# Performance work log

Hardware: AMD Instinct MI355X
Metric: run time of the kernel (lower is better)

Reference implementation:

```python
import jax, jax.numpy as jnp
import numpy as np

B, S0, S1 = 4, 768, 256
T = S0 + S1
D0, D1 = 2048, 1024
N, K, H = 8, 1, 256  # num_heads, num_kv_heads, head_dim
G = N // K
BIG_NEG = -2.3819763e38


def _apply_rope(x, positions, max_wavelength=10000):
    # x: [B, L, Hn, Hd]; positions: [B, L] float32
    half = x.shape[-1] // 2
    freq_exponents = (2.0 / x.shape[-1]) * jnp.arange(half, dtype=jnp.float32)
    timescale = max_wavelength ** freq_exponents
    radians = positions[..., None] / timescale[None, None, :]   # [B, L, half]
    radians = radians[..., None, :]                             # [B, L, 1, half]
    sin, cos = jnp.sin(radians), jnp.cos(radians)
    x1, x2 = jnp.split(x, 2, axis=-1)
    res = jnp.concatenate([x1 * cos - x2 * sin, x2 * cos + x1 * sin], axis=-1)
    return res.astype(x.dtype)


def setup_inputs() -> dict:
    key = jax.random.key(0)
    ks = jax.random.split(key, 8)
    x0 = jax.random.normal(ks[0], (B, S0, D0), dtype=jnp.float32)
    x1 = jax.random.normal(ks[1], (B, S1, D1), dtype=jnp.float32)
    positions = jnp.broadcast_to(jnp.arange(T, dtype=jnp.float32), (B, T))
    # causal mask [B, 1, T, T]
    attn_mask = jnp.broadcast_to(jnp.tril(jnp.ones((T, T), dtype=bool)), (B, 1, T, T))
    # lecun_normal-style init: std = 1/sqrt(fan_in=width)
    q0_w = jax.random.normal(ks[2], (N, D0, H), dtype=jnp.float32) * (D0 ** -0.5)
    kv0_w = jax.random.normal(ks[3], (2, K, D0, H), dtype=jnp.float32) * (D0 ** -0.5)
    q1_w = jax.random.normal(ks[4], (N, D1, H), dtype=jnp.float32) * (D1 ** -0.5)
    kv1_w = jax.random.normal(ks[5], (2, K, D1, H), dtype=jnp.float32) * (D1 ** -0.5)
    o0_w = jax.random.normal(ks[6], (N, H, D0), dtype=jnp.float32) * ((N * H) ** -0.5)
    o1_w = jax.random.normal(ks[7], (N, H, D1), dtype=jnp.float32) * ((N * H) ** -0.5)
    return {"x0": x0, "x1": x1, "positions": positions, "attn_mask": attn_mask,
            "q0_w": q0_w, "kv0_w": kv0_w, "q1_w": q1_w, "kv1_w": kv1_w,
            "o0_w": o0_w, "o1_w": o1_w}


def reference(x0, x1, positions, attn_mask, q0_w, kv0_w, q1_w, kv1_w, o0_w, o1_w):
    dtype = x0.dtype
    # per-stream GQA projections (num_kv_heads != num_heads path)
    q_a = jnp.einsum('BTD,NDH->BTNH', x0, q0_w)
    kv_a = jnp.einsum('BSD,CKDH->CBSKH', x0, kv0_w)
    q_b = jnp.einsum('BTD,NDH->BTNH', x1, q1_w)
    kv_b = jnp.einsum('BSD,CKDH->CBSKH', x1, kv1_w)
    # concat streams along sequence
    q = jnp.concatenate([q_a, q_b], axis=1)                 # [B, T, N, H]
    k = jnp.concatenate([kv_a[0], kv_b[0]], axis=1)         # [B, T, K, H]
    v = jnp.concatenate([kv_a[1], kv_b[1]], axis=1)         # [B, T, K, H]
    # inline RoPE + query scaling
    q = _apply_rope(q, positions) * (H ** -0.5)
    k = _apply_rope(k, positions)
    # GQA grouping: N = K * G
    qg = q.reshape(q.shape[0], q.shape[1], K, G, H)          # [B, T, K, G, H]
    logits = jnp.einsum('BTKGH,BSKH->BKGTS', qg, k,
                        preferred_element_type=jnp.float32)  # fp32 scores
    masked = jnp.where(attn_mask[:, :, None, :, :], logits, BIG_NEG)
    probs = jax.nn.softmax(masked, axis=-1).astype(dtype)
    encoded = jnp.einsum('BKGTS,BSKH->BTKGH', probs, v)
    encoded = encoded.reshape(encoded.shape[0], encoded.shape[1], N, H)  # [B, T, N, H]
    out0 = jnp.einsum('BTNH,NHD->BTD', encoded[:, :S0], o0_w)
    out1 = jnp.einsum('BTNH,NHD->BTD', encoded[:, S0:], o1_w)
    return (out0, out1)
```

## Files before the change

kernel.cpp:

```cpp
#include <hip/hip_runtime.h>

typedef unsigned short u16;
typedef __attribute__((ext_vector_type(8))) short bf16x8;
typedef __attribute__((ext_vector_type(4))) float f32x4;

#define CB   4
#define CS0  768
#define CS1  256
#define CT   1024
#define CD0  2048
#define CD1  1024
#define CN   8
#define CH   256
#define IDENT (1 << 30)
#define BIGBASE 0x7fffffff

__device__ __forceinline__ float bf2f(u16 u) {
    union { unsigned int i; float f; } v;
    v.i = ((unsigned int)u) << 16;
    return v.f;
}
__device__ __forceinline__ u16 f2bf(float f) {
    union { float f; unsigned int i; } v;
    v.f = f;
    unsigned int r = 0x7fffu + ((v.i >> 16) & 1u);
    return (u16)((v.i + r) >> 16);
}

__device__ __forceinline__ void gl_lds16(const u16* g, u16* lds_base) {
    __builtin_amdgcn_global_load_lds(
        (const __attribute__((address_space(1))) void*)g,
        (__attribute__((address_space(3))) void*)lds_base,
        16, 0, 0);
}

struct PSeg { const float* in; u16* out; int R, C, base, lgx, lgy, mode; };
struct PSeg8 { PSeg t[8]; };

__global__ __launch_bounds__(256) void prep_multi(PSeg8 segs)
{
    __shared__ float tl[32][33];
    int bid = blockIdx.x;
    PSeg g = segs.t[0];
    #pragma unroll
    for (int i = 1; i < 8; i++)
        if (bid >= segs.t[i].base) g = segs.t[i];
    int r = bid - g.base;
    if (g.mode == 0) {
        int i = r * 256 + threadIdx.x;
        float4 v = ((const float4*)g.in)[i];
        ushort4 o;
        o.x = f2bf(v.x); o.y = f2bf(v.y); o.z = f2bf(v.z); o.w = f2bf(v.w);
        ((ushort4*)g.out)[i] = o;
    } else {
        int bx = r & ((1 << g.lgx) - 1);
        int by = (r >> g.lgx) & ((1 << g.lgy) - 1);
        int bz = r >> (g.lgx + g.lgy);
        const float* in = g.in + (size_t)bz * g.R * g.C;
        u16* out = g.out + (size_t)bz * g.R * g.C;
        int c0 = bx * 32, r0 = by * 32;
        int tx = threadIdx.x & 31, ty = threadIdx.x >> 5;
        #pragma unroll
        for (int i = 0; i < 32; i += 8)
            tl[ty + i][tx] = in[(size_t)(r0 + ty + i) * g.C + c0 + tx];
        __syncthreads();
        #pragma unroll
        for (int i = 0; i < 32; i += 8)
            out[(size_t)(c0 + ty + i) * g.R + r0 + tx] = f2bf(tl[tx][ty + i]);
    }
}

struct GSeg {
    const u16* A; const u16* BT; void* C;
    int K, Cstride, base, lgnx;
    int Sa, Ta, ta, Sc, Tc, tc, obf, pad;
};
struct GSeg4 { GSeg s[4]; };

__global__ __launch_bounds__(256) void mfma_gemm_multi(GSeg4 segs)
{
    __shared__ u16 As[128 * 32];
    __shared__ u16 Bs[128 * 32];

    int bid = blockIdx.x;
    GSeg g = segs.s[0];
    if (bid >= segs.s[1].base) g = segs.s[1];
    if (bid >= segs.s[2].base) g = segs.s[2];
    if (bid >= segs.s[3].base) g = segs.s[3];

    int tid  = threadIdx.x;
    int r    = bid - g.base;
    int n0   = (r & ((1 << g.lgnx) - 1)) * 128;
    int m0   = (r >> g.lgnx) * 128;
    int wave = tid >> 6, lane = tid & 63;

    int srow  = tid >> 2;
    int skoff = ((tid & 3) ^ ((srow >> 1) & 3)) * 8;
    int am1 = m0 + srow, am2 = m0 + 64 + srow;
    const u16* aptr1 = g.A + (size_t)((am1 / g.Sa) * g.Ta + g.ta + am1 % g.Sa) * g.K + skoff;
    const u16* aptr2 = g.A + (size_t)((am2 / g.Sa) * g.Ta + g.ta + am2 % g.Sa) * g.K + skoff;
    const u16* bptr1 = g.BT + (size_t)(n0 + srow) * g.K + skoff;
    const u16* bptr2 = g.BT + (size_t)(n0 + 64 + srow) * g.K + skoff;

    int mw = (wave >> 1) * 64, nw = (wave & 1) * 64;
    int lrow = lane & 15;
    int q4   = lane >> 4;
    int sw   = (q4 ^ ((lrow >> 1) & 3)) * 8;

    f32x4 acc[4][4] = {};

    for (int k0 = 0; k0 < g.K; k0 += 32) {
        gl_lds16(aptr1 + k0, As + wave * 512);
        gl_lds16(aptr2 + k0, As + 2048 + wave * 512);
        gl_lds16(bptr1 + k0, Bs + wave * 512);
        gl_lds16(bptr2 + k0, Bs + 2048 + wave * 512);
        __syncthreads();
        bf16x8 af[4], bfr[4];
        #pragma unroll
        for (int i = 0; i < 4; i++)
            af[i] = *(const bf16x8*)&As[(mw + i * 16 + lrow) * 32 + sw];
        #pragma unroll
        for (int i = 0; i < 4; i++)
            bfr[i] = *(const bf16x8*)&Bs[(nw + i * 16 + lrow) * 32 + sw];
        #pragma unroll
        for (int mi = 0; mi < 4; mi++)
            #pragma unroll
            for (int ni = 0; ni < 4; ni++)
                acc[mi][ni] = __builtin_amdgcn_mfma_f32_16x16x32_bf16(
                    af[mi], bfr[ni], acc[mi][ni], 0, 0, 0);
        __syncthreads();
    }

    #pragma unroll
    for (int mi = 0; mi < 4; mi++) {
        #pragma unroll
        for (int rr = 0; rr < 4; rr++) {
            int mm = m0 + mw + mi * 16 + q4 * 4 + rr;
            int grow = (mm / g.Sc) * g.Tc + g.tc + mm % g.Sc;
            if (g.obf) {
                u16* crow = (u16*)g.C + (size_t)grow * g.Cstride + n0 + nw + lrow;
                #pragma unroll
                for (int ni = 0; ni < 4; ni++)
                    crow[ni * 16] = f2bf(acc[mi][ni][rr]);
            } else {
                float* crow = (float*)g.C + (size_t)grow * g.Cstride + n0 + nw + lrow;
                #pragma unroll
                for (int ni = 0; ni < 4; ni++)
                    crow[ni * 16] = acc[mi][ni][rr];
            }
        }
    }
}

__global__ __launch_bounds__(256) void rope_vt_kernel(
    const u16* __restrict__ qsrc, const u16* __restrict__ kvsrc,
    const float* __restrict__ positions,
    u16* __restrict__ qb, u16* __restrict__ kb, u16* __restrict__ vto)
{
    int bid = blockIdx.x;
    if (bid < 18432) {
        int idx = bid * 256 + threadIdx.x;
        const int QP = CB * CT * CN * 128;
        if (idx < QP) {
            int h  = idx & 127;
            int n  = (idx >> 7) & 7;
            int bt = idx >> 10;
            const u16* base = qsrc + (size_t)bt * 2048 + n * 256;
            float pos = positions[bt];
            float ts  = powf(10000.0f, (float)h * (1.0f / 128.0f));
            float rr  = pos / ts;
            float sn = sinf(rr), cs = cosf(rr);
            float x1 = bf2f(base[h]), x2 = bf2f(base[h + 128]);
            u16* ob = qb + (size_t)bt * 2048 + n * 256;
            ob[h]       = f2bf((x1 * cs - x2 * sn) * 0.0625f);
            ob[h + 128] = f2bf((x2 * cs + x1 * sn) * 0.0625f);
        } else {
            int j  = idx - QP;
            int h  = j & 127;
            int bt = j >> 7;
            const u16* base = kvsrc + (size_t)bt * 512;
            float pos = positions[bt];
            float ts  = powf(10000.0f, (float)h * (1.0f / 128.0f));
            float rr  = pos / ts;
            float sn = sinf(rr), cs = cosf(rr);
            float x1 = bf2f(base[h]), x2 = bf2f(base[h + 128]);
            int b = bt >> 10, t = bt & 1023;
            int h2 = h + 128;
            kb[((size_t)(b * 8 + (h  >> 5)) * 1024 + t) * 32 + (h  & 31)] = f2bf(x1 * cs - x2 * sn);
            kb[((size_t)(b * 8 + (h2 >> 5)) * 1024 + t) * 32 + (h2 & 31)] = f2bf(x2 * cs + x1 * sn);
        }
    } else {
        int vb = bid - 18432;
        int h  = threadIdx.x;
        int sc = vb & 31;
        int b  = vb >> 5;
        const u16* src = kvsrc + ((size_t)(b * 1024 + sc * 32) * 512 + 256 + h);
        u16* dst = vto + ((size_t)(b * 32 + sc) * 256 + h) * 32;
        u16 buf[32];
        #pragma unroll
        for (int ss = 0; ss < 32; ss++)
            buf[ss] = src[(size_t)ss * 512];
        #pragma unroll
        for (int i = 0; i < 8; i++)
            ((ushort4*)dst)[i] = ((ushort4*)buf)[i];
    }
}

__global__ __launch_bounds__(256) void flash_attn(
    const u16* __restrict__ qb, const u16* __restrict__ kb,
    const u16* __restrict__ vt, u16* __restrict__ encoded)
{
    __shared__ __align__(16) u16 Ks[8 * 64 * 32];
    __shared__ __align__(16) u16 Vs[2 * 256 * 32];
    __shared__ __align__(16) u16 Pw[4][16 * 72];

    int tid  = threadIdx.x;
    int wave = tid >> 6, lane = tid & 63;
    int q4 = lane >> 4, l15 = lane & 15;
    int swz = (q4 ^ ((l15 >> 1) & 3)) * 8;

    int bid  = blockIdx.x;
    int half = bid >> 8;
    int r    = bid & 255;
    int b    = (half << 1) | (r >> 7);
    int ti   = r & 127;
    if (half) ti = 127 - ti;
    int t0 = ti * 8;

    bf16x8 af[8];
    {
        int m = wave * 16 + l15;
        int head = m >> 3, tl = m & 7;
        const u16* qrow = qb + ((size_t)(b * CT + t0 + tl) * 2048 + head * 256 + q4 * 8);
        #pragma unroll
        for (int kc = 0; kc < 8; kc++)
            af[kc] = *(const bf16x8*)(qrow + kc * 32);
    }

    f32x4 O[16] = {};
    float lrun[4] = {0.f, 0.f, 0.f, 0.f};

    int send = t0 + 8;
    for (int s0 = 0; s0 < send; s0 += 64) {
        bool lastTile = (s0 + 64 >= send);
        if (s0) __syncthreads();
        #pragma unroll
        for (int is = 0; is < 8; is++) {
            int ubase = is * 256 + wave * 64;
            int u = ubase + lane;
            int s = (u >> 2) & 63, hc = u >> 8;
            int ug = (u & 3) ^ ((s >> 1) & 3);
            const u16* g = kb + ((size_t)((b * 8 + hc) * 1024 + s0 + s) * 32 + ug * 8);
            gl_lds16(g, Ks + (size_t)ubase * 8);
        }
        #pragma unroll
        for (int is = 0; is < 8; is++) {
            int ubase = is * 256 + wave * 64;
            int u = ubase + lane;
            int h = (u >> 2) & 255;
            int vg = (u & 3) ^ ((h >> 1) & 3);
            const u16* g = vt + ((size_t)(b * 32 + (s0 >> 5)) * 8192 + (size_t)(u >> 2) * 32 + vg * 8);
            gl_lds16(g, Vs + (size_t)ubase * 8);
        }
        __syncthreads();

        f32x4 P[4];
        #pragma unroll
        for (int ni = 0; ni < 4; ni++) {
            f32x4 c = {};
            #pragma unroll
            for (int kc = 0; kc < 8; kc++) {
                bf16x8 bfr = *(const bf16x8*)&Ks[kc * 2048 + (ni * 16 + l15) * 32 + swz];
                c = __builtin_amdgcn_mfma_f32_16x16x32_bf16(af[kc], bfr, c, 0, 0, 0);
            }
            P[ni] = c;
        }

        if (lastTile) {
            #pragma unroll
            for (int ni = 0; ni < 4; ni++)
                #pragma unroll
                for (int rr = 0; rr < 4; rr++) {
                    int trow = t0 + ((q4 * 4 + rr) & 7);
                    int scol = s0 + ni * 16 + l15;
                    if (scol > trow) P[ni][rr] = -3.0e38f;
                }
        }

        #pragma unroll
        for (int ni = 0; ni < 4; ni++)
            #pragma unroll
            for (int rr = 0; rr < 4; rr++) {
                float e = __expf(P[ni][rr]);
                P[ni][rr] = e;
                Pw[wave][(q4 * 4 + rr) * 72 + ni * 16 + l15] = f2bf(e);
            }
        #pragma unroll
        for (int rr = 0; rr < 4; rr++) {
            float s = (P[0][rr] + P[1][rr]) + (P[2][rr] + P[3][rr]);
            s += __shfl_xor(s, 1);
            s += __shfl_xor(s, 2);
            s += __shfl_xor(s, 4);
            s += __shfl_xor(s, 8);
            lrun[rr] += s;
        }

        bf16x8 pa0 = *(const bf16x8*)&Pw[wave][l15 * 72 + q4 * 8];
        bf16x8 pa1 = *(const bf16x8*)&Pw[wave][l15 * 72 + 32 + q4 * 8];
        #pragma unroll
        for (int nc = 0; nc < 16; nc++) {
            bf16x8 b0 = *(const bf16x8*)&Vs[(nc * 16 + l15) * 32 + swz];
            bf16x8 b1 = *(const bf16x8*)&Vs[8192 + (nc * 16 + l15) * 32 + swz];
            O[nc] = __builtin_amdgcn_mfma_f32_16x16x32_bf16(pa0, b0, O[nc], 0, 0, 0);
            O[nc] = __builtin_amdgcn_mfma_f32_16x16x32_bf16(pa1, b1, O[nc], 0, 0, 0);
        }
    }

    #pragma unroll
    for (int rr = 0; rr < 4; rr++) {
        int mm = wave * 16 + q4 * 4 + rr;
        int hd = mm >> 3, tl = mm & 7;
        u16* erow = encoded + ((size_t)(b * CT + t0 + tl) * 2048 + hd * 256 + l15);
        float inv = 1.0f / lrun[rr];
        #pragma unroll
        for (int nc = 0; nc < 16; nc++)
            erow[nc * 16] = f2bf(O[nc][rr] * inv);
    }
}

extern "C" void kernel_launch(void* const* d_in, const int* in_sizes, int n_in,
                              void* d_out, int out_size, void* d_ws, size_t ws_size,
                              hipStream_t stream)
{
    const float* x0        = (const float*)d_in[0];
    const float* x1        = (const float*)d_in[1];
    const float* positions = (const float*)d_in[2];
    const float* q0_w  = (const float*)d_in[4];
    const float* kv0_w = (const float*)d_in[5];
    const float* q1_w  = (const float*)d_in[6];
    const float* kv1_w = (const float*)d_in[7];
    const float* o0_w  = (const float*)d_in[8];
    const float* o1_w  = (const float*)d_in[9];
    float* out = (float*)d_out;

    char* W = (char*)d_ws;
    u16* qbuf16  = (u16*)(W);
    u16* kvbuf16 = (u16*)(W + 16777216);
    u16* WTo0  = (u16*)(W + 20971520);
    u16* WTo1  = (u16*)(W + 29360128);
    u16* x0b   = (u16*)(W + 33554432);
    u16* x1b   = (u16*)(W + 46137344);
    u16* WTq0  = (u16*)(W + 48234496);
    u16* WTkv0 = (u16*)(W + 56623104);
    u16* WTq1  = (u16*)(W + 58720256);
    u16* WTkv1 = (u16*)(W + 62914560);
    u16* qb  = x0b;
    u16* kb  = WTkv0;
    u16* vtb = WTq1;
    u16* encoded = qbuf16;

    PSeg8 ps8;
    ps8.t[0] = { x0,    x0b,      0,    0,     0, 0, 0, 0 };
    ps8.t[1] = { x1,    x1b,      0,    0,  6144, 0, 0, 0 };
    ps8.t[2] = { q0_w,  WTq0,  2048,  256,  7168, 3, 6, 1 };
    ps8.t[3] = { kv0_w, WTkv0, 2048,  256, 11264, 3, 6, 1 };
    ps8.t[4] = { q1_w,  WTq1,  1024,  256, 12288, 3, 5, 1 };
    ps8.t[5] = { kv1_w, WTkv1, 1024,  256, 14336, 3, 5, 1 };
    ps8.t[6] = { o0_w,  WTo0,  2048, 2048, 14848, 6, 6, 1 };
    ps8.t[7] = { o1_w,  WTo1,  2048, 1024, 18944, 5, 6, 1 };
    prep_multi<<<dim3(20992), dim3(256), 0, stream>>>(ps8);

    GSeg4 ps;
    ps.s[0] = { x0b, WTq0,  qbuf16,  2048, 2048,   0, 4, IDENT, 0, 0, CS0, CT, 0,   1, 0 };
    ps.s[1] = { x0b, WTkv0, kvbuf16, 2048,  512, 384, 2, IDENT, 0, 0, CS0, CT, 0,   1, 0 };
    ps.s[2] = { x1b, WTq1,  qbuf16,  1024, 2048, 480, 4, IDENT, 0, 0, CS1, CT, CS0, 1, 0 };
    ps.s[3] = { x1b, WTkv1, kvbuf16, 1024,  512, 608, 2, IDENT, 0, 0, CS1, CT, CS0, 1, 0 };
    mfma_gemm_multi<<<dim3(640), dim3(256), 0, stream>>>(ps);

    rope_vt_kernel<<<dim3(18560), dim3(256), 0, stream>>>(
        qbuf16, kvbuf16, positions, qb, kb, vtb);

    flash_attn<<<dim3(512), dim3(256), 0, stream>>>(qb, kb, vtb, encoded);

    GSeg4 os;
    os.s[0] = { encoded, WTo0, out, 2048, 2048,   0, 4, CS0, CT, 0,   IDENT, 0, 0, 0, 0 };
    os.s[1] = { encoded, WTo1, out + (size_t)CB * CS0 * CD0,
                2048, 1024, 384, 3, CS1, CT, CS0, IDENT, 0, 0, 0, 0 };
    os.s[2] = { nullptr, nullptr, nullptr, 0, 0, BIGBASE, 0, 1, 0, 0, 1, 0, 0, 0, 0 };
    os.s[3] = { nullptr, nullptr, nullptr, 0, 0, BIGBASE, 0, 1, 0, 0, 1, 0, 0, 0, 0 };
    mfma_gemm_multi<<<dim3(448), dim3(256), 0, stream>>>(os);
}
```

Before: 330.0 us.

## Fuse all stages into one persistent kernel with grid barriers

Replaces the five separate launches (convert/transpose, QKV GEMM, RoPE/V-transpose, flash attention, output GEMM) with a single persistent kernel of 512 blocks. The blocks loop over each stage's work items and synchronise through a software grid barrier in workspace memory. It also precomputes the RoPE timescales in LDS, switches to fast sin/cos intrinsics, and remaps GEMM tile order. The intent is to remove launch gaps and tail effects between stages. In exchange, the barriers serialise all blocks, shared memory is sized for the largest stage which may cap occupancy, and co-residency of all 512 blocks is assumed.

```diff
diff --git a/kernel.cpp b/kernel.cpp
--- a/kernel.cpp
+++ b/kernel.cpp
@@ -10,10 +10,9 @@
 #define CT   1024
 #define CD0  2048
 #define CD1  1024
-#define CN   8
-#define CH   256
 #define IDENT (1 << 30)
-#define BIGBASE 0x7fffffff
+#define NBLK 512u
+#define BAR_OFF (64u * 1024u * 1024u)
 
 __device__ __forceinline__ float bf2f(u16 u) {
     union { unsigned int i; float f; } v;
@@ -26,7 +25,6 @@
     unsigned int r = 0x7fffu + ((v.i >> 16) & 1u);
     return (u16)((v.i + r) >> 16);
 }
-
 __device__ __forceinline__ void gl_lds16(const u16* g, u16* lds_base) {
     __builtin_amdgcn_global_load_lds(
         (const __attribute__((address_space(1))) void*)g,
@@ -34,73 +32,50 @@
         16, 0, 0);
 }
 
-struct PSeg { const float* in; u16* out; int R, C, base, lgx, lgy, mode; };
-struct PSeg8 { PSeg t[8]; };
-
-__global__ __launch_bounds__(256) void prep_multi(PSeg8 segs)
+__device__ __forceinline__ void grid_barrier(unsigned* bar) {
+    __syncthreads();
+    __threadfence();
+    if (threadIdx.x == 0) {
+        unsigned* cnt = bar;
+        unsigned* gen = bar + 16;
+        unsigned g = __hip_atomic_load(gen, __ATOMIC_RELAXED, __HIP_MEMORY_SCOPE_AGENT);
+        unsigned a = __hip_atomic_fetch_add(cnt, 1u, __ATOMIC_ACQ_REL, __HIP_MEMORY_SCOPE_AGENT);
+        if (a == NBLK - 1u) {
+            __hip_atomic_store(cnt, 0u, __ATOMIC_RELAXED, __HIP_MEMORY_SCOPE_AGENT);
+            __hip_atomic_store(gen, g + 1u, __ATOMIC_RELEASE, __HIP_MEMORY_SCOPE_AGENT);
+        } else {
+            while (__hip_atomic_load(gen, __ATOMIC_ACQUIRE, __HIP_MEMORY_SCOPE_AGENT) == g)
+                __builtin_amdgcn_s_sleep(2);
+        }
+    }
+    __syncthreads();
+    __threadfence();
+}
+
+struct KArgs {
+    const float *x0, *x1, *positions, *q0w, *kv0w, *q1w, *kv1w, *o0w, *o1w;
+    float* out;
+    u16 *x0b, *x1b, *WTq0, *WTkv0, *WTq1, *WTkv1, *WTo0, *WTo1;
+    u16 *qbuf16, *kvbuf16;
+    unsigned* bar;
+};
+
+__device__ __forceinline__ void gemm_tile(
+    const u16* __restrict__ A, const u16* __restrict__ BT, void* C, int obf,
+    int K, int Cstride, int m0, int n0,
+    int Sa, int Ta, int ta, int Sc, int Tc, int tc,
+    u16* As, u16* Bs)
 {
-    __shared__ float tl[32][33];
-    int bid = blockIdx.x;
-    PSeg g = segs.t[0];
-    #pragma unroll
-    for (int i = 1; i < 8; i++)
-        if (bid >= segs.t[i].base) g = segs.t[i];
-    int r = bid - g.base;
-    if (g.mode == 0) {
-        int i = r * 256 + threadIdx.x;
-        float4 v = ((const float4*)g.in)[i];
-        ushort4 o;
-        o.x = f2bf(v.x); o.y = f2bf(v.y); o.z = f2bf(v.z); o.w = f2bf(v.w);
-        ((ushort4*)g.out)[i] = o;
-    } else {
-        int bx = r & ((1 << g.lgx) - 1);
-        int by = (r >> g.lgx) & ((1 << g.lgy) - 1);
-        int bz = r >> (g.lgx + g.lgy);
-        const float* in = g.in + (size_t)bz * g.R * g.C;
-        u16* out = g.out + (size_t)bz * g.R * g.C;
-        int c0 = bx * 32, r0 = by * 32;
-        int tx = threadIdx.x & 31, ty = threadIdx.x >> 5;
-        #pragma unroll
-        for (int i = 0; i < 32; i += 8)
-            tl[ty + i][tx] = in[(size_t)(r0 + ty + i) * g.C + c0 + tx];
-        __syncthreads();
-        #pragma unroll
-        for (int i = 0; i < 32; i += 8)
-            out[(size_t)(c0 + ty + i) * g.R + r0 + tx] = f2bf(tl[tx][ty + i]);
-    }
-}
-
-struct GSeg {
-    const u16* A; const u16* BT; void* C;
-    int K, Cstride, base, lgnx;
-    int Sa, Ta, ta, Sc, Tc, tc, obf, pad;
-};
-struct GSeg4 { GSeg s[4]; };
-
-__global__ __launch_bounds__(256) void mfma_gemm_multi(GSeg4 segs)
-{
-    __shared__ u16 As[128 * 32];
-    __shared__ u16 Bs[128 * 32];
-
-    int bid = blockIdx.x;
-    GSeg g = segs.s[0];
-    if (bid >= segs.s[1].base) g = segs.s[1];
-    if (bid >= segs.s[2].base) g = segs.s[2];
-    if (bid >= segs.s[3].base) g = segs.s[3];
-
     int tid  = threadIdx.x;
-    int r    = bid - g.base;
-    int n0   = (r & ((1 << g.lgnx) - 1)) * 128;
-    int m0   = (r >> g.lgnx) * 128;
     int wave = tid >> 6, lane = tid & 63;
 
     int srow  = tid >> 2;
     int skoff = ((tid & 3) ^ ((srow >> 1) & 3)) * 8;
     int am1 = m0 + srow, am2 = m0 + 64 + srow;
-    const u16* aptr1 = g.A + (size_t)((am1 / g.Sa) * g.Ta + g.ta + am1 % g.Sa) * g.K + skoff;
-    const u16* aptr2 = g.A + (size_t)((am2 / g.Sa) * g.Ta + g.ta + am2 % g.Sa) * g.K + skoff;
-    const u16* bptr1 = g.BT + (size_t)(n0 + srow) * g.K + skoff;
-    const u16* bptr2 = g.BT + (size_t)(n0 + 64 + srow) * g.K + skoff;
+    const u16* aptr1 = A + (size_t)((am1 / Sa) * Ta + ta + am1 % Sa) * K + skoff;
+    const u16* aptr2 = A + (size_t)((am2 / Sa) * Ta + ta + am2 % Sa) * K + skoff;
+    const u16* bptr1 = BT + (size_t)(n0 + srow) * K + skoff;
+    const u16* bptr2 = BT + (size_t)(n0 + 64 + srow) * K + skoff;
 
     int mw = (wave >> 1) * 64, nw = (wave & 1) * 64;
     int lrow = lane & 15;
@@ -109,7 +84,7 @@
 
     f32x4 acc[4][4] = {};
 
-    for (int k0 = 0; k0 < g.K; k0 += 32) {
+    for (int k0 = 0; k0 < K; k0 += 32) {
         gl_lds16(aptr1 + k0, As + wave * 512);
         gl_lds16(aptr2 + k0, As + 2048 + wave * 512);
         gl_lds16(bptr1 + k0, Bs + wave * 512);
@@ -136,14 +111,14 @@
         #pragma unroll
         for (int rr = 0; rr < 4; rr++) {
             int mm = m0 + mw + mi * 16 + q4 * 4 + rr;
-            int grow = (mm / g.Sc) * g.Tc + g.tc + mm % g.Sc;
-            if (g.obf) {
-                u16* crow = (u16*)g.C + (size_t)grow * g.Cstride + n0 + nw + lrow;
+            int grow = (mm / Sc) * Tc + tc + mm % Sc;
+            if (obf) {
+                u16* crow = (u16*)C + (size_t)grow * Cstride + n0 + nw + lrow;
                 #pragma unroll
                 for (int ni = 0; ni < 4; ni++)
                     crow[ni * 16] = f2bf(acc[mi][ni][rr]);
             } else {
-                float* crow = (float*)g.C + (size_t)grow * g.Cstride + n0 + nw + lrow;
+                float* crow = (float*)C + (size_t)grow * Cstride + n0 + nw + lrow;
                 #pragma unroll
                 for (int ni = 0; ni < 4; ni++)
                     crow[ni * 16] = acc[mi][ni][rr];
@@ -152,179 +127,268 @@
     }
 }
 
-__global__ __launch_bounds__(256) void rope_vt_kernel(
-    const u16* __restrict__ qsrc, const u16* __restrict__ kvsrc,
-    const float* __restrict__ positions,
-    u16* __restrict__ qb, u16* __restrict__ kb, u16* __restrict__ vto)
+__device__ __forceinline__ void tile_coords(int r, int nt, int mt, int& m0, int& n0)
 {
+    int wr = (r & 7) * (nt >> 3) + (r >> 3);
+    m0 = (wr % mt) * 128;
+    n0 = (wr / mt) * 128;
+}
+
+__global__ __launch_bounds__(256, 2) void mega(KArgs a)
+{
+    __shared__ __align__(16) char smem[74752];
+    int tid = threadIdx.x;
     int bid = blockIdx.x;
-    if (bid < 18432) {
-        int idx = bid * 256 + threadIdx.x;
-        const int QP = CB * CT * CN * 128;
-        if (idx < QP) {
-            int h  = idx & 127;
-            int n  = (idx >> 7) & 7;
-            int bt = idx >> 10;
-            const u16* base = qsrc + (size_t)bt * 2048 + n * 256;
-            float pos = positions[bt];
-            float ts  = powf(10000.0f, (float)h * (1.0f / 128.0f));
-            float rr  = pos / ts;
-            float sn = sinf(rr), cs = cosf(rr);
-            float x1 = bf2f(base[h]), x2 = bf2f(base[h + 128]);
-            u16* ob = qb + (size_t)bt * 2048 + n * 256;
-            ob[h]       = f2bf((x1 * cs - x2 * sn) * 0.0625f);
-            ob[h + 128] = f2bf((x2 * cs + x1 * sn) * 0.0625f);
-        } else {
-            int j  = idx - QP;
-            int h  = j & 127;
-            int bt = j >> 7;
-            const u16* base = kvsrc + (size_t)bt * 512;
-            float pos = positions[bt];
-            float ts  = powf(10000.0f, (float)h * (1.0f / 128.0f));
-            float rr  = pos / ts;
-            float sn = sinf(rr), cs = cosf(rr);
-            float x1 = bf2f(base[h]), x2 = bf2f(base[h + 128]);
-            int b = bt >> 10, t = bt & 1023;
-            int h2 = h + 128;
-            kb[((size_t)(b * 8 + (h  >> 5)) * 1024 + t) * 32 + (h  & 31)] = f2bf(x1 * cs - x2 * sn);
-            kb[((size_t)(b * 8 + (h2 >> 5)) * 1024 + t) * 32 + (h2 & 31)] = f2bf(x2 * cs + x1 * sn);
-        }
-    } else {
-        int vb = bid - 18432;
-        int h  = threadIdx.x;
-        int sc = vb & 31;
-        int b  = vb >> 5;
-        const u16* src = kvsrc + ((size_t)(b * 1024 + sc * 32) * 512 + 256 + h);
-        u16* dst = vto + ((size_t)(b * 32 + sc) * 256 + h) * 32;
-        u16 buf[32];
-        #pragma unroll
-        for (int ss = 0; ss < 32; ss++)
-            buf[ss] = src[(size_t)ss * 512];
-        #pragma unroll
-        for (int i = 0; i < 8; i++)
-            ((ushort4*)dst)[i] = ((ushort4*)buf)[i];
-    }
-}
-
-__global__ __launch_bounds__(256) void flash_attn(
-    const u16* __restrict__ qb, const u16* __restrict__ kb,
-    const u16* __restrict__ vt, u16* __restrict__ encoded)
-{
-    __shared__ __align__(16) u16 Ks[8 * 64 * 32];
-    __shared__ __align__(16) u16 Vs[2 * 256 * 32];
-    __shared__ __align__(16) u16 Pw[4][16 * 72];
-
-    int tid  = threadIdx.x;
-    int wave = tid >> 6, lane = tid & 63;
-    int q4 = lane >> 4, l15 = lane & 15;
-    int swz = (q4 ^ ((l15 >> 1) & 3)) * 8;
-
-    int bid  = blockIdx.x;
-    int half = bid >> 8;
-    int r    = bid & 255;
-    int b    = (half << 1) | (r >> 7);
-    int ti   = r & 127;
-    if (half) ti = 127 - ti;
-    int t0 = ti * 8;
-
-    bf16x8 af[8];
+
     {
-        int m = wave * 16 + l15;
-        int head = m >> 3, tl = m & 7;
-        const u16* qrow = qb + ((size_t)(b * CT + t0 + tl) * 2048 + head * 256 + q4 * 8);
-        #pragma unroll
-        for (int kc = 0; kc < 8; kc++)
-            af[kc] = *(const bf16x8*)(qrow + kc * 32);
-    }
-
-    f32x4 O[16] = {};
-    float lrun[4] = {0.f, 0.f, 0.f, 0.f};
-
-    int send = t0 + 8;
-    for (int s0 = 0; s0 < send; s0 += 64) {
-        bool lastTile = (s0 + 64 >= send);
-        if (s0) __syncthreads();
-        #pragma unroll
-        for (int is = 0; is < 8; is++) {
-            int ubase = is * 256 + wave * 64;
-            int u = ubase + lane;
-            int s = (u >> 2) & 63, hc = u >> 8;
-            int ug = (u & 3) ^ ((s >> 1) & 3);
-            const u16* g = kb + ((size_t)((b * 8 + hc) * 1024 + s0 + s) * 32 + ug * 8);
-            gl_lds16(g, Ks + (size_t)ubase * 8);
-        }
-        #pragma unroll
-        for (int is = 0; is < 8; is++) {
-            int ubase = is * 256 + wave * 64;
-            int u = ubase + lane;
-            int h = (u >> 2) & 255;
-            int vg = (u & 3) ^ ((h >> 1) & 3);
-            const u16* g = vt + ((size_t)(b * 32 + (s0 >> 5)) * 8192 + (size_t)(u >> 2) * 32 + vg * 8);
-            gl_lds16(g, Vs + (size_t)ubase * 8);
-        }
+        float (*tl)[33] = (float(*)[33])smem;
+        for (int u = bid; u < 20992; u += NBLK) {
+            const float* in; u16* outp; int R=0, C=0, lgx=0, lgy=0, mode, base;
+            if      (u <  6144) { in=a.x0;   outp=a.x0b;   mode=0; base=0; }
+            else if (u <  7168) { in=a.x1;   outp=a.x1b;   mode=0; base=6144; }
+            else if (u < 11264) { in=a.q0w;  outp=a.WTq0;  R=2048; C=256;  lgx=3; lgy=6; mode=1; base=7168; }
+            else if (u < 12288) { in=a.kv0w; outp=a.WTkv0; R=2048; C=256;  lgx=3; lgy=6; mode=1; base=11264; }
+            else if (u < 14336) { in=a.q1w;  outp=a.WTq1;  R=1024; C=256;  lgx=3; lgy=5; mode=1; base=12288; }
+            else if (u < 14848) { in=a.kv1w; outp=a.WTkv1; R=1024; C=256;  lgx=3; lgy=5; mode=1; base=14336; }
+            else if (u < 18944) { in=a.o0w;  outp=a.WTo0;  R=2048; C=2048; lgx=6; lgy=6; mode=1; base=14848; }
+            else                { in=a.o1w;  outp=a.WTo1;  R=2048; C=1024; lgx=5; lgy=6; mode=1; base=18944; }
+            int r = u - base;
+            if (mode == 0) {
+                int i = r * 256 + tid;
+                float4 v = ((const float4*)in)[i];
+                ushort4 o;
+                o.x = f2bf(v.x); o.y = f2bf(v.y); o.z = f2bf(v.z); o.w = f2bf(v.w);
+                ((ushort4*)outp)[i] = o;
+            } else {
+                int bx = r & ((1 << lgx) - 1);
+                int by = (r >> lgx) & ((1 << lgy) - 1);
+                int bz = r >> (lgx + lgy);
+                const float* inz = in + (size_t)bz * R * C;
+                u16* outz = outp + (size_t)bz * R * C;
+                int c0 = bx * 32, r0 = by * 32;
+                int tx = tid & 31, ty = tid >> 5;
+                __syncthreads();
+                #pragma unroll
+                for (int i = 0; i < 32; i += 8)
+                    tl[ty + i][tx] = inz[(size_t)(r0 + ty + i) * C + c0 + tx];
+                __syncthreads();
+                #pragma unroll
+                for (int i = 0; i < 32; i += 8)
+                    outz[(size_t)(c0 + ty + i) * R + r0 + tx] = f2bf(tl[tx][ty + i]);
+            }
+        }
+    }
+    grid_barrier(a.bar);
+
+    {
+        u16* As = (u16*)smem;
+        u16* Bs = (u16*)(smem + 8192);
+        for (int t = bid; t < 640; t += NBLK) {
+            const u16 *A, *BT; u16* C; int K, Cst, base, nt, mt, Sc, Tc, tc;
+            if      (t < 384) { A=a.x0b; BT=a.WTq0;  C=a.qbuf16;  K=2048; Cst=2048; base=0;   nt=384; mt=24; Sc=CS0; Tc=CT; tc=0; }
+            else if (t < 480) { A=a.x0b; BT=a.WTkv0; C=a.kvbuf16; K=2048; Cst=512;  base=384; nt=96;  mt=24; Sc=CS0; Tc=CT; tc=0; }
+            else if (t < 608) { A=a.x1b; BT=a.WTq1;  C=a.qbuf16;  K=1024; Cst=2048; base=480; nt=128; mt=8;  Sc=CS1; Tc=CT; tc=CS0; }
+            else              { A=a.x1b; BT=a.WTkv1; C=a.kvbuf16; K=1024; Cst=512;  base=608; nt=32;  mt=8;  Sc=CS1; Tc=CT; tc=CS0; }
+            int m0, n0;
+            tile_coords(t - base, nt, mt, m0, n0);
+            gemm_tile(A, BT, C, 1, K, Cst, m0, n0, IDENT, 0, 0, Sc, Tc, tc, As, Bs);
+        }
+    }
+    grid_barrier(a.bar);
+
+    {
+        float* tstab = (float*)smem;
+        if (tid < 128) tstab[tid] = powf(10000.0f, (float)tid * (1.0f / 128.0f));
         __syncthreads();
-
-        f32x4 P[4];
-        #pragma unroll
-        for (int ni = 0; ni < 4; ni++) {
-            f32x4 c = {};
-            #pragma unroll
-            for (int kc = 0; kc < 8; kc++) {
-                bf16x8 bfr = *(const bf16x8*)&Ks[kc * 2048 + (ni * 16 + l15) * 32 + swz];
-                c = __builtin_amdgcn_mfma_f32_16x16x32_bf16(af[kc], bfr, c, 0, 0, 0);
-            }
-            P[ni] = c;
-        }
-
-        if (lastTile) {
+        const u16* qsrc  = a.qbuf16;
+        const u16* kvsrc = a.kvbuf16;
+        u16* qb  = a.x0b;
+        u16* kb  = a.WTkv0;
+        u16* vto = a.WTq1;
+        for (int u = bid; u < 18560; u += NBLK) {
+            if (u < 18432) {
+                int idx = u * 256 + tid;
+                const int QP = CB * CT * 8 * 128;
+                if (idx < QP) {
+                    int h  = idx & 127;
+                    int n  = (idx >> 7) & 7;
+                    int bt = idx >> 10;
+                    const u16* base = qsrc + (size_t)bt * 2048 + n * 256;
+                    float pos = a.positions[bt];
+                    float rr  = pos / tstab[h];
+                    float sn = __sinf(rr), cs = __cosf(rr);
+                    float x1 = bf2f(base[h]), x2 = bf2f(base[h + 128]);
+                    u16* ob = qb + (size_t)bt * 2048 + n * 256;
+                    ob[h]       = f2bf((x1 * cs - x2 * sn) * 0.0625f);
+                    ob[h + 128] = f2bf((x2 * cs + x1 * sn) * 0.0625f);
+                } else {
+                    int j  = idx - QP;
+                    int h  = j & 127;
+                    int bt = j >> 7;
+                    const u16* base = kvsrc + (size_t)bt * 512;
+                    float pos = a.positions[bt];
+                    float rr  = pos / tstab[h];
+                    float sn = __sinf(rr), cs = __cosf(rr);
+                    float x1 = bf2f(base[h]), x2 = bf2f(base[h + 128]);
+                    int b = bt >> 10, t = bt & 1023;
+                    int h2 = h + 128;
+                    kb[((size_t)(b * 8 + (h  >> 5)) * 1024 + t) * 32 + (h  & 31)] = f2bf(x1 * cs - x2 * sn);
+                    kb[((size_t)(b * 8 + (h2 >> 5)) * 1024 + t) * 32 + (h2 & 31)] = f2bf(x2 * cs + x1 * sn);
+                }
+            } else {
+                int vb = u - 18432;
+                int h  = tid;
+                int sc = vb & 31;
+                int b  = vb >> 5;
+                const u16* src = kvsrc + ((size_t)(b * 1024 + sc * 32) * 512 + 256 + h);
+                u16* dst = vto + ((size_t)(b * 32 + sc) * 256 + h) * 32;
+                u16 buf[32];
+                #pragma unroll
+                for (int ss = 0; ss < 32; ss++)
+                    buf[ss] = src[(size_t)ss * 512];
+                #pragma unroll
+                for (int i = 0; i < 8; i++)
+                    ((ushort4*)dst)[i] = ((ushort4*)buf)[i];
+            }
+        }
+    }
+    grid_barrier(a.bar);
+
+    {
+        u16* Ks = (u16*)smem;
+        u16* Vs = (u16*)(smem + 32768);
+        u16* Pw = (u16*)(smem + 65536);
+        const u16* qb = a.x0b;
+        const u16* kb = a.WTkv0;
+        const u16* vt = a.WTq1;
+        u16* encoded  = a.qbuf16;
+
+        int wave = tid >> 6, lane = tid & 63;
+        int q4 = lane >> 4, l15 = lane & 15;
+        int swz = (q4 ^ ((l15 >> 1) & 3)) * 8;
+        u16* Pwp = Pw + wave * 1152;
+
+        int half = bid >> 8;
+        int r    = bid & 255;
+        int b    = (half << 1) | (r >> 7);
+        int ti   = r & 127;
+        if (half) ti = 127 - ti;
+        int t0 = ti * 8;
+
+        bf16x8 af[8];
+        {
+            int m = wave * 16 + l15;
+            int head = m >> 3, tl = m & 7;
+            const u16* qrow = qb + ((size_t)(b * CT + t0 + tl) * 2048 + head * 256 + q4 * 8);
+            #pragma unroll
+            for (int kc = 0; kc < 8; kc++)
+                af[kc] = *(const bf16x8*)(qrow + kc * 32);
+        }
+
+        f32x4 O[16] = {};
+        float lrun[4] = {0.f, 0.f, 0.f, 0.f};
+
+        int send = t0 + 8;
+        for (int s0 = 0; s0 < send; s0 += 64) {
+            bool lastTile = (s0 + 64 >= send);
+            __syncthreads();
+            #pragma unroll
+            for (int is = 0; is < 8; is++) {
+                int ubase = is * 256 + wave * 64;
+                int u = ubase + lane;
+                int s = (u >> 2) & 63, hc = u >> 8;
+                int ug = (u & 3) ^ ((s >> 1) & 3);
+                const u16* g = kb + ((size_t)((b * 8 + hc) * 1024 + s0 + s) * 32 + ug * 8);
+                gl_lds16(g, Ks + (size_t)ubase * 8);
+            }
+            #pragma unroll
+            for (int is = 0; is < 8; is++) {
+                int ubase = is * 256 + wave * 64;
+                int u = ubase + lane;
+                int h = (u >> 2) & 255;
+                int vg = (u & 3) ^ ((h >> 1) & 3);
+                const u16* g = vt + ((size_t)(b * 32 + (s0 >> 5)) * 8192 + (size_t)(u >> 2) * 32 + vg * 8);
+                gl_lds16(g, Vs + (size_t)ubase * 8);
+            }
+            __syncthreads();
+
+            f32x4 P[4];
+            #pragma unroll
+            for (int ni = 0; ni < 4; ni++) {
+                f32x4 c = {};
+                #pragma unroll
+                for (int kc = 0; kc < 8; kc++) {
+                    bf16x8 bfr = *(const bf16x8*)&Ks[kc * 2048 + (ni * 16 + l15) * 32 + swz];
+                    c = __builtin_amdgcn_mfma_f32_16x16x32_bf16(af[kc], bfr, c, 0, 0, 0);
+                }
+                P[ni] = c;
+            }
+
+            if (lastTile) {
+                #pragma unroll
+                for (int ni = 0; ni < 4; ni++)
+                    #pragma unroll
+                    for (int rr = 0; rr < 4; rr++) {
+                        int trow = t0 + ((q4 * 4 + rr) & 7);
+                        int scol = s0 + ni * 16 + l15;
+                        if (scol > trow) P[ni][rr] = -3.0e38f;
+                    }
+            }
+
             #pragma unroll
             for (int ni = 0; ni < 4; ni++)
                 #pragma unroll
                 for (int rr = 0; rr < 4; rr++) {
-                    int trow = t0 + ((q4 * 4 + rr) & 7);
-                    int scol = s0 + ni * 16 + l15;
-                    if (scol > trow) P[ni][rr] = -3.0e38f;
+                    float e = __expf(P[ni][rr]);
+                    P[ni][rr] = e;
+                    Pwp[(q4 * 4 + rr) * 72 + ni * 16 + l15] = f2bf(e);
                 }
-        }
-
-        #pragma unroll
-        for (int ni = 0; ni < 4; ni++)
             #pragma unroll
             for (int rr = 0; rr < 4; rr++) {
-                float e = __expf(P[ni][rr]);
-                P[ni][rr] = e;
-                Pw[wave][(q4 * 4 + rr) * 72 + ni * 16 + l15] = f2bf(e);
-            }
+                float s = (P[0][rr] + P[1][rr]) + (P[2][rr] + P[3][rr]);
+                s += __shfl_xor(s, 1);
+                s += __shfl_xor(s, 2);
+                s += __shfl_xor(s, 4);
+                s += __shfl_xor(s, 8);
+                lrun[rr] += s;
+            }
+
+            bf16x8 pa0 = *(const bf16x8*)&Pwp[l15 * 72 + q4 * 8];
+            bf16x8 pa1 = *(const bf16x8*)&Pwp[l15 * 72 + 32 + q4 * 8];
+            #pragma unroll
+            for (int nc = 0; nc < 16; nc++) {
+                bf16x8 b0 = *(const bf16x8*)&Vs[(nc * 16 + l15) * 32 + swz];
+                bf16x8 b1 = *(const bf16x8*)&Vs[8192 + (nc * 16 + l15) * 32 + swz];
+                O[nc] = __builtin_amdgcn_mfma_f32_16x16x32_bf16(pa0, b0, O[nc], 0, 0, 0);
+                O[nc] = __builtin_amdgcn_mfma_f32_16x16x32_bf16(pa1, b1, O[nc], 0, 0, 0);
+            }
+        }
+
         #pragma unroll
         for (int rr = 0; rr < 4; rr++) {
-            float s = (P[0][rr] + P[1][rr]) + (P[2][rr] + P[3][rr]);
-            s += __shfl_xor(s, 1);
-            s += __shfl_xor(s, 2);
-            s += __shfl_xor(s, 4);
-            s += __shfl_xor(s, 8);
-            lrun[rr] += s;
-        }
-
-        bf16x8 pa0 = *(const bf16x8*)&Pw[wave][l15 * 72 + q4 * 8];
-        bf16x8 pa1 = *(const bf16x8*)&Pw[wave][l15 * 72 + 32 + q4 * 8];
-        #pragma unroll
-        for (int nc = 0; nc < 16; nc++) {
-            bf16x8 b0 = *(const bf16x8*)&Vs[(nc * 16 + l15) * 32 + swz];
-            bf16x8 b1 = *(const bf16x8*)&Vs[8192 + (nc * 16 + l15) * 32 + swz];
-            O[nc] = __builtin_amdgcn_mfma_f32_16x16x32_bf16(pa0, b0, O[nc], 0, 0, 0);
-            O[nc] = __builtin_amdgcn_mfma_f32_16x16x32_bf16(pa1, b1, O[nc], 0, 0, 0);
-        }
-    }
-
-    #pragma unroll
-    for (int rr = 0; rr < 4; rr++) {
-        int mm = wave * 16 + q4 * 4 + rr;
-        int hd = mm >> 3, tl = mm & 7;
-        u16* erow = encoded + ((size_t)(b * CT + t0 + tl) * 2048 + hd * 256 + l15);
-        float inv = 1.0f / lrun[rr];
-        #pragma unroll
-        for (int nc = 0; nc < 16; nc++)
-            erow[nc * 16] = f2bf(O[nc][rr] * inv);
+            int mm = wave * 16 + q4 * 4 + rr;
+            int hd = mm >> 3, tl = mm & 7;
+            u16* erow = encoded + ((size_t)(b * CT + t0 + tl) * 2048 + hd * 256 + l15);
+            float inv = 1.0f / lrun[rr];
+            #pragma unroll
+            for (int nc = 0; nc < 16; nc++)
+                erow[nc * 16] = f2bf(O[nc][rr] * inv);
+        }
+    }
+    grid_barrier(a.bar);
+
+    {
+        u16* As = (u16*)smem;
+        u16* Bs = (u16*)(smem + 8192);
+        const u16* encoded = a.qbuf16;
+        for (int t = bid; t < 448; t += NBLK) {
+            const u16* BT; float* C; int Cst, base, nt, mt, Sa, Ta, ta;
+            if (t < 384) { BT=a.WTo0; C=a.out;                               Cst=2048; base=0;   nt=384; mt=24; Sa=CS0; Ta=CT; ta=0; }
+            else         { BT=a.WTo1; C=a.out + (size_t)CB * CS0 * CD0;      Cst=1024; base=384; nt=64;  mt=8;  Sa=CS1; Ta=CT; ta=CS0; }
+            int m0, n0;
+            tile_coords(t - base, nt, mt, m0, n0);
+            gemm_tile(encoded, BT, C, 0, 2048, Cst, m0, n0, Sa, Ta, ta, IDENT, 0, 0, As, Bs);
+        }
     }
 }
 
@@ -332,61 +396,31 @@
                               void* d_out, int out_size, void* d_ws, size_t ws_size,
                               hipStream_t stream)
 {
-    const float* x0        = (const float*)d_in[0];
-    const float* x1        = (const float*)d_in[1];
-    const float* positions = (const float*)d_in[2];
-    const float* q0_w  = (const float*)d_in[4];
-    const float* kv0_w = (const float*)d_in[5];
-    const float* q1_w  = (const float*)d_in[6];
-    const float* kv1_w = (const float*)d_in[7];
-    const float* o0_w  = (const float*)d_in[8];
-    const float* o1_w  = (const float*)d_in[9];
-    float* out = (float*)d_out;
-
     char* W = (char*)d_ws;
-    u16* qbuf16  = (u16*)(W);
-    u16* kvbuf16 = (u16*)(W + 16777216);
-    u16* WTo0  = (u16*)(W + 20971520);
-    u16* WTo1  = (u16*)(W + 29360128);
-    u16* x0b   = (u16*)(W + 33554432);
-    u16* x1b   = (u16*)(W + 46137344);
-    u16* WTq0  = (u16*)(W + 48234496);
-    u16* WTkv0 = (u16*)(W + 56623104);
-    u16* WTq1  = (u16*)(W + 58720256);
-    u16* WTkv1 = (u16*)(W + 62914560);
-    u16* qb  = x0b;
-    u16* kb  = WTkv0;
-    u16* vtb = WTq1;
-    u16* encoded = qbuf16;
-
-    PSeg8 ps8;
-    ps8.t[0] = { x0,    x0b,      0,    0,     0, 0, 0, 0 };
-    ps8.t[1] = { x1,    x1b,      0,    0,  6144, 0, 0, 0 };
-    ps8.t[2] = { q0_w,  WTq0,  2048,  256,  7168, 3, 6, 1 };
-    ps8.t[3] = { kv0_w, WTkv0, 2048,  256, 11264, 3, 6, 1 };
-    ps8.t[4] = { q1_w,  WTq1,  1024,  256, 12288, 3, 5, 1 };
-    ps8.t[5] = { kv1_w, WTkv1, 1024,  256, 14336, 3, 5, 1 };
-    ps8.t[6] = { o0_w,  WTo0,  2048, 2048, 14848, 6, 6, 1 };
-    ps8.t[7] = { o1_w,  WTo1,  2048, 1024, 18944, 5, 6, 1 };
-    prep_multi<<<dim3(20992), dim3(256), 0, stream>>>(ps8);
-
-    GSeg4 ps;
-    ps.s[0] = { x0b, WTq0,  qbuf16,  2048, 2048,   0, 4, IDENT, 0, 0, CS0, CT, 0,   1, 0 };
-    ps.s[1] = { x0b, WTkv0, kvbuf16, 2048,  512, 384, 2, IDENT, 0, 0, CS0, CT, 0,   1, 0 };
-    ps.s[2] = { x1b, WTq1,  qbuf16,  1024, 2048, 480, 4, IDENT, 0, 0, CS1, CT, CS0, 1, 0 };
-    ps.s[3] = { x1b, WTkv1, kvbuf16, 1024,  512, 608, 2, IDENT, 0, 0, CS1, CT, CS0, 1, 0 };
-    mfma_gemm_multi<<<dim3(640), dim3(256), 0, stream>>>(ps);
-
-    rope_vt_kernel<<<dim3(18560), dim3(256), 0, stream>>>(
-        qbuf16, kvbuf16, positions, qb, kb, vtb);
-
-    flash_attn<<<dim3(512), dim3(256), 0, stream>>>(qb, kb, vtb, encoded);
-
-    GSeg4 os;
-    os.s[0] = { encoded, WTo0, out, 2048, 2048,   0, 4, CS0, CT, 0,   IDENT, 0, 0, 0, 0 };
-    os.s[1] = { encoded, WTo1, out + (size_t)CB * CS0 * CD0,
-                2048, 1024, 384, 3, CS1, CT, CS0, IDENT, 0, 0, 0, 0 };
-    os.s[2] = { nullptr, nullptr, nullptr, 0, 0, BIGBASE, 0, 1, 0, 0, 1, 0, 0, 0, 0 };
-    os.s[3] = { nullptr, nullptr, nullptr, 0, 0, BIGBASE, 0, 1, 0, 0, 1, 0, 0, 0, 0 };
-    mfma_gemm_multi<<<dim3(448), dim3(256), 0, stream>>>(os);
-}
+    KArgs ka;
+    ka.x0  = (const float*)d_in[0];
+    ka.x1  = (const float*)d_in[1];
+    ka.positions = (const float*)d_in[2];
+    ka.q0w  = (const float*)d_in[4];
+    ka.kv0w = (const float*)d_in[5];
+    ka.q1w  = (const float*)d_in[6];
+    ka.kv1w = (const float*)d_in[7];
+    ka.o0w  = (const float*)d_in[8];
+    ka.o1w  = (const float*)d_in[9];
+    ka.out  = (float*)d_out;
+
+    ka.qbuf16  = (u16*)(W);
+    ka.kvbuf16 = (u16*)(W + 16777216);
+    ka.WTo0  = (u16*)(W + 20971520);
+    ka.WTo1  = (u16*)(W + 29360128);
+    ka.x0b   = (u16*)(W + 33554432);
+    ka.x1b   = (u16*)(W + 46137344);
+    ka.WTq0  = (u16*)(W + 48234496);
+    ka.WTkv0 = (u16*)(W + 56623104);
+    ka.WTq1  = (u16*)(W + 58720256);
+    ka.WTkv1 = (u16*)(W + 62914560);
+    ka.bar   = (unsigned*)(W + BAR_OFF);
+
+    hipMemsetAsync(W + BAR_OFF, 0, 128, stream);
+    mega<<<dim3(NBLK), dim3(256), 0, stream>>>(ka);
+}
```

New measurement: 1.134 ms. +243.6%, slower.
